# Performance work log

Measured on AMD Instinct MI355X. Metric: run time of the kernel, lower is better.

## Reference

```python
import jax, jax.numpy as jnp
import numpy as np

H = 16      # num_heads
HD = 64     # head_dim
W = 1024    # local window size
G = 256     # number of global tokens
EPS = 1e-6
NEG = -1e30


def setup_inputs() -> dict:
    key = jax.random.key(0)
    ks = jax.random.split(key, 7)
    B, S, D = 1, 8192, 1024
    inner = H * HD
    s = 0.02
    return {
        "x": jax.random.normal(ks[0], (B, S, D), jnp.float32),
        "norm_w": jnp.ones((D,), jnp.float32),
        "w_q": jax.random.normal(ks[1], (D, inner), jnp.float32) * s,
        "w_k": jax.random.normal(ks[2], (D, inner), jnp.float32) * s,
        "w_v": jax.random.normal(ks[3], (D, inner), jnp.float32) * s,
        "w_out": jax.random.normal(ks[4], (inner, D), jnp.float32) * s,
        "scorer_w": jax.random.normal(ks[5], (D, 1), jnp.float32) * s,
        "scorer_b": jnp.zeros((1,), jnp.float32),
    }


def reference(x, norm_w, w_q, w_k, w_v, w_out, scorer_w, scorer_b):
    B, S, D = x.shape
    # pre-norm (RMSNorm)
    h = x * jax.lax.rsqrt(jnp.mean(x * x, axis=-1, keepdims=True) + EPS) * norm_w

    def proj(w):  # [B,S,D] -> [B,H,S,HD]
        return jnp.einsum('bsd,de->bse', h, w).reshape(B, S, H, HD).transpose(0, 2, 1, 3)

    q, k, v = proj(w_q), proj(w_k), proj(w_v)
    scale = HD ** -0.5

    # --- local block attention (non-overlapping causal windows) ---
    nW = S // W
    qw = q.reshape(B, H, nW, W, HD)
    kw = k.reshape(B, H, nW, W, HD)
    vw = v.reshape(B, H, nW, W, HD)
    ll = jnp.einsum('bhnqd,bhnkd->bhnqk', qw, kw) * scale  # [B,H,nW,W,W]
    cm = jnp.tril(jnp.ones((W, W), bool))
    ll = jnp.where(cm, ll, NEG).reshape(B, H, S, W)

    # --- sparse global attention over top-G important tokens ---
    scores = (jnp.einsum('bsd,do->bso', h, scorer_w) + scorer_b)[..., 0]  # [B,S]
    _, idx = jax.lax.top_k(scores, G)                                     # [B,G]
    kg = jnp.take_along_axis(k, idx[:, None, :, None], axis=2)            # [B,H,G,HD]
    vg = jnp.take_along_axis(v, idx[:, None, :, None], axis=2)
    lg = jnp.einsum('bhsd,bhgd->bhsg', q, kg) * scale                     # [B,H,S,G]
    pos = jnp.arange(S)
    gmask = idx[:, None, None, :] <= pos[None, None, :, None]             # causal: global pos <= query pos
    lg = jnp.where(gmask, lg, NEG)

    # --- joint softmax over local window + global tokens ---
    attn = jax.nn.softmax(jnp.concatenate([ll, lg], axis=-1), axis=-1)    # [B,H,S,W+G]
    a_loc = attn[..., :W].reshape(B, H, nW, W, W)
    o = jnp.einsum('bhnqk,bhnkd->bhnqd', a_loc, vw).reshape(B, H, S, HD)
    o = o + jnp.einsum('bhsg,bhgd->bhsd', attn[..., W:], vg)

    o = o.transpose(0, 2, 1, 3).reshape(B, S, H * HD)
    return x + jnp.einsum('bse,ed->bsd', o, w_out)  # residual
```

## Files before the change

kernel.cpp:

```cpp
#include <hip/hip_runtime.h>
#include <stdint.h>

#define S_LEN 8192
#define DIM   1024
#define NH    16
#define HD    64
#define WIN   1024
#define GTOK  256
#define QKV_STRIDE (3 * DIM)

typedef __attribute__((ext_vector_type(8))) short bf16x8;
typedef __attribute__((ext_vector_type(4))) float f32x4;
typedef __attribute__((ext_vector_type(16))) float f32x16;
typedef unsigned short u16;
typedef uint32_t u32;

__device__ __forceinline__ u16 f2bf(float f) {
  union { float f; uint32_t u; } v; v.f = f;
  uint32_t r = v.u + 0x7fffu + ((v.u >> 16) & 1u);
  return (u16)(r >> 16);
}
__device__ __forceinline__ float bf2f(u16 b) {
  union { uint32_t u; float f; } v; v.u = ((uint32_t)b) << 16;
  return v.f;
}
__device__ __forceinline__ uint32_t cvtpk(float a, float b) {
  uint32_t r;
  asm("v_cvt_pk_bf16_f32 %0, %1, %2" : "=v"(r) : "v"(a), "v"(b));
  return r;
}

__device__ __forceinline__ void gload_lds16(const void* g, void* l) {
  __builtin_amdgcn_global_load_lds((const __attribute__((address_space(1))) void*)g,
                                   (__attribute__((address_space(3))) void*)l, 16, 0, 0);
}

__global__ __launch_bounds__(256) void rmsnorm_score_kernel(
    const float* __restrict__ x, const float* __restrict__ nw,
    const float* __restrict__ sw, const float* __restrict__ sb,
    u16* __restrict__ h, float* __restrict__ scores) {
  int row = blockIdx.x, tid = threadIdx.x;
  const float4* xr = (const float4*)(x + (size_t)row * DIM);
  float4 v = xr[tid];
  float ss = v.x * v.x + v.y * v.y + v.z * v.z + v.w * v.w;
#pragma unroll
  for (int o = 32; o >= 1; o >>= 1) ss += __shfl_xor(ss, o);
  __shared__ float red[4], red2[4];
  int wv = tid >> 6;
  if ((tid & 63) == 0) red[wv] = ss;
  __syncthreads();
  ss = red[0] + red[1] + red[2] + red[3];
  float rn = rsqrtf(ss * (1.0f / DIM) + 1e-6f);
  float4 w4 = ((const float4*)nw)[tid];
  float h0 = v.x * rn * w4.x, h1 = v.y * rn * w4.y;
  float h2 = v.z * rn * w4.z, h3 = v.w * rn * w4.w;
  uint64_t pack = (uint64_t)f2bf(h0) | ((uint64_t)f2bf(h1) << 16) |
                  ((uint64_t)f2bf(h2) << 32) | ((uint64_t)f2bf(h3) << 48);
  *(uint64_t*)(h + (size_t)row * DIM + tid * 4) = pack;
  float4 s4 = ((const float4*)sw)[tid];
  float sc = h0 * s4.x + h1 * s4.y + h2 * s4.z + h3 * s4.w;
#pragma unroll
  for (int o = 32; o >= 1; o >>= 1) sc += __shfl_xor(sc, o);
  if ((tid & 63) == 0) red2[wv] = sc;
  __syncthreads();
  if (tid == 0) scores[row] = red2[0] + red2[1] + red2[2] + red2[3] + sb[0];
}

__global__ __launch_bounds__(256) void transpose_w_kernel(
    const float* __restrict__ wq, const float* __restrict__ wk,
    const float* __restrict__ wv, const float* __restrict__ wo,
    u16* __restrict__ wqkvT, u16* __restrict__ woutT) {
  __shared__ float tile[32][33];
  int z = blockIdx.z;
  const float* src = (z == 0) ? wq : (z == 1) ? wk : (z == 2) ? wv : wo;
  u16* dst = (z < 3) ? (wqkvT + (size_t)z * DIM * DIM) : woutT;
  int tx = threadIdx.x, ty = threadIdx.y;
  int n0 = blockIdx.x * 32, k0 = blockIdx.y * 32;
#pragma unroll
  for (int i = 0; i < 4; i++)
    tile[ty + i * 8][tx] = src[(size_t)(k0 + ty + i * 8) * DIM + n0 + tx];
  __syncthreads();
#pragma unroll
  for (int i = 0; i < 4; i++)
    dst[(size_t)(n0 + ty + i * 8) * DIM + k0 + tx] = f2bf(tile[tx][ty + i * 8]);
}

__global__ __launch_bounds__(256) void topk_init_kernel(int* __restrict__ cnt) {
  cnt[blockIdx.x * 256 + threadIdx.x] = 0;
}

__global__ __launch_bounds__(256) void topk_count_kernel(
    const float* __restrict__ scores, int* __restrict__ cnt) {
  __shared__ float sj[1024];
  int jbase = blockIdx.y * 1024;
  for (int t = threadIdx.x; t < 1024; t += 256) sj[t] = scores[jbase + t];
  __syncthreads();
  int i = blockIdx.x * 256 + threadIdx.x;
  float my = scores[i];
  int c = 0;
  const float4* s4 = (const float4*)sj;
#pragma unroll 4
  for (int j = 0; j < 256; j++) {
    float4 v = s4[j];
    int b = jbase + j * 4;
    c += (v.x > my) || (v.x == my && (b + 0) < i);
    c += (v.y > my) || (v.y == my && (b + 1) < i);
    c += (v.z > my) || (v.z == my && (b + 2) < i);
    c += (v.w > my) || (v.w == my && (b + 3) < i);
  }
  if (c) atomicAdd(&cnt[i], c);
}

__global__ __launch_bounds__(256) void topk_scatter_kernel(
    const int* __restrict__ cnt, int* __restrict__ gidx) {
  int i = blockIdx.x * 256 + threadIdx.x;
  int c = cnt[i];
  if (c < GTOK) gidx[c] = i;
}

__global__ __launch_bounds__(128) void gather_kernel(
    const u16* __restrict__ qkv, const int* __restrict__ gidx,
    u16* __restrict__ kg, u16* __restrict__ vg) {
  int g = blockIdx.x, t = threadIdx.x;
  size_t src = (size_t)gidx[g] * QKV_STRIDE;
  *(bf16x8*)(kg + (size_t)g * DIM + t * 8) = *(const bf16x8*)(qkv + src + DIM + t * 8);
  *(bf16x8*)(vg + (size_t)g * DIM + t * 8) = *(const bf16x8*)(qkv + src + 2 * DIM + t * 8);
}

template <int RESID>
__global__ __launch_bounds__(512, 2) void gemm256_kernel(
    const u16* __restrict__ A, const u16* __restrict__ B,
    u16* __restrict__ Cb, float* __restrict__ Cf, const float* __restrict__ X,
    int M, int N, int K) {
  __shared__ __align__(16) u16 As[3][256 * 64];
  __shared__ __align__(16) u16 Bs[3][128 * 64];
  const int tid = threadIdx.x;
  const int wave = tid >> 6, lane = tid & 63;
  const int l15 = lane & 15, l4 = lane >> 4;
  const int wr = wave >> 1, wc = wave & 1;
  const int mbase = blockIdx.x * 256, nbase = blockIdx.y * 128;
  const int srow = lane >> 3, schunk = lane & 7;
  const int gcol = (schunk ^ srow) * 8;

  auto stage = [&](int tt, int b) {
    const int kt = tt << 6;
#pragma unroll
    for (int l = 0; l < 4; l++) {
      int row = wave * 32 + l * 8;
      gload_lds16(A + (size_t)(mbase + row + srow) * K + kt + gcol, &As[b][row * 64]);
    }
#pragma unroll
    for (int l = 0; l < 2; l++) {
      int row = wave * 16 + l * 8;
      gload_lds16(B + (size_t)(nbase + row + srow) * K + kt + gcol, &Bs[b][row * 64]);
    }
  };

  const int nt = K >> 6;
  f32x4 acc[4][4] = {};

  stage(0, 0);
  stage(1, 1);
  asm volatile("s_waitcnt vmcnt(6)" ::: "memory");
  __builtin_amdgcn_s_barrier();
  __builtin_amdgcn_sched_barrier(0);

  int cur = 0;
  for (int t = 0; t < nt; t++) {
    int pre = cur + 2; if (pre >= 3) pre -= 3;
    if (t + 2 < nt) stage(t + 2, pre);
    const u16* Ab = &As[cur][0];
    const u16* Bb = &Bs[cur][0];
    bf16x8 bfr[4][2], af[4][2];
#pragma unroll
    for (int nf = 0; nf < 4; nf++) {
      int row = wc * 64 + nf * 16 + l15;
#pragma unroll
      for (int kk = 0; kk < 2; kk++)
        bfr[nf][kk] = *(const bf16x8*)(Bb + row * 64 + (((kk * 4 + l4) ^ (l15 & 7)) * 8));
    }
#pragma unroll
    for (int mi = 0; mi < 4; mi++) {
      int row = wr * 64 + mi * 16 + l15;
#pragma unroll
      for (int kk = 0; kk < 2; kk++)
        af[mi][kk] = *(const bf16x8*)(Ab + row * 64 + (((kk * 4 + l4) ^ (l15 & 7)) * 8));
    }
    __builtin_amdgcn_s_setprio(1);
#pragma unroll
    for (int mi = 0; mi < 4; mi++)
#pragma unroll
      for (int nf = 0; nf < 4; nf++)
#pragma unroll
        for (int kk = 0; kk < 2; kk++)
          acc[mi][nf] = __builtin_amdgcn_mfma_f32_16x16x32_bf16(af[mi][kk], bfr[nf][kk],
                                                                acc[mi][nf], 0, 0, 0);
    __builtin_amdgcn_s_setprio(0);
    if (t + 1 < nt) {
      if (t + 2 < nt) asm volatile("s_waitcnt vmcnt(6)" ::: "memory");
      else            asm volatile("s_waitcnt vmcnt(0)" ::: "memory");
      __builtin_amdgcn_s_barrier();
      __builtin_amdgcn_sched_barrier(0);
    }
    cur = (cur + 1 == 3) ? 0 : cur + 1;
  }

#pragma unroll
  for (int mi = 0; mi < 4; mi++) {
#pragma unroll
    for (int nf = 0; nf < 4; nf++) {
#pragma unroll
      for (int r = 0; r < 4; r++) {
        int row = mbase + wr * 64 + mi * 16 + l4 * 4 + r;
        int col = nbase + wc * 64 + nf * 16 + l15;
        float v = acc[mi][nf][r];
        if (RESID) Cf[(size_t)row * N + col] = X[(size_t)row * N + col] + v;
        else       Cb[(size_t)row * N + col] = f2bf(v);
      }
    }
  }
}

__global__ __launch_bounds__(512) void attn_kernel(
    const u16* __restrict__ qkv, const u16* __restrict__ kg,
    const u16* __restrict__ vg, const int* __restrict__ gidx,
    u16* __restrict__ o) {
  __shared__ __align__(16) u16 kT[2][64][72];
  __shared__ __align__(16) u16 vT[2][64][72];
  __shared__ int gposLds[2][64];
  const int tid = threadIdx.x, wave = tid >> 6, lane = tid & 63;
  const int l31 = lane & 31, hi = lane >> 5;

  const int r = blockIdx.x + 32 * blockIdx.y;
  const int half = r >> 8, rr = r & 255;
  const int h = rr >> 4, w8 = rr & 7, jj = (rr >> 3) & 1;
  const int j = half ? (jj ? 1 : 0) : (jj ? 2 : 3);
  const int wbase = w8 * WIN;
  const int hoff = h * HD;
  const int qsbase = wbase + j * 256;
  const int nLocal = (j + 1) * 4;
  const int nTiles = nLocal + GTOK / 64;
  const int qrow = qsbase + wave * 32 + l31;
  const int qwmax = qsbase + wave * 32 + 31;

  const int skey = tid >> 3, sd8 = (tid & 7) * 8;
  const int vcol = skey ^ ((sd8 >> 4) << 4);

  bf16x8 qf[4];
  {
    const float SC2 = 0.125f * 1.44269504088896f;
    const u16* qptr = qkv + (size_t)qrow * QKV_STRIDE + hoff + hi * 8;
#pragma unroll
    for (int ks = 0; ks < 4; ks++) {
      bf16x8 raw = *(const bf16x8*)(qptr + ks * 16);
      bf16x8 sc;
#pragma unroll
      for (int t = 0; t < 8; t++) sc[t] = (short)f2bf(bf2f((u16)raw[t]) * SC2);
      qf[ks] = sc;
    }
  }

  bf16x8 nk, nv;
  int ng = 0;
  {
    const u16* base = qkv + (size_t)(wbase + skey) * QKV_STRIDE + hoff + sd8;
    nk = *(const bf16x8*)(base + DIM);
    nv = *(const bf16x8*)(base + 2 * DIM);
  }

  f32x16 acc0 = {}, acc1 = {};
  float mr = -3.0e38f, lr = 0.f;

  for (int t = 0; t < nTiles; t++) {
    const int p = t & 1;
    const bool isLocal = (t < nLocal);
    const int tbase = wbase + t * 64;
    *(bf16x8*)(&kT[p][skey][sd8]) = nk;
#pragma unroll
    for (int t8 = 0; t8 < 8; t8++) vT[p][sd8 + t8][vcol] = (u16)nv[t8];
    if (!isLocal && tid < 64) gposLds[p][tid] = ng;
    {
      const int nt = t + 1;
      const u16 *ksrc = nullptr, *vsrc = nullptr;
      if (nt < nLocal) {
        const u16* base = qkv + (size_t)(wbase + nt * 64 + skey) * QKV_STRIDE + hoff + sd8;
        ksrc = base + DIM; vsrc = base + 2 * DIM;
      } else if (nt < nTiles) {
        size_t grow = (size_t)((nt - nLocal) * 64 + skey) * DIM + hoff + sd8;
        ksrc = kg + grow; vsrc = vg + grow;
        if (tid < 64) ng = gidx[(nt - nLocal) * 64 + tid];
      }
      if (ksrc) { nk = *(const bf16x8*)(ksrc); nv = *(const bf16x8*)(vsrc); }
    }
    asm volatile("s_waitcnt lgkmcnt(0)" ::: "memory");
    __builtin_amdgcn_s_barrier();
    __builtin_amdgcn_sched_barrier(0);

    if (isLocal && tbase > qwmax) continue;

    float sv[32];
    __builtin_amdgcn_s_setprio(1);
#pragma unroll
    for (int kb = 0; kb < 2; kb++) {
      const u16* krow = &kT[p][kb * 32 + l31][hi * 8];
      bf16x8 k0 = *(const bf16x8*)(krow);
      bf16x8 k1 = *(const bf16x8*)(krow + 16);
      bf16x8 k2 = *(const bf16x8*)(krow + 32);
      bf16x8 k3 = *(const bf16x8*)(krow + 48);
      f32x16 z = {};
      z = __builtin_amdgcn_mfma_f32_32x32x16_bf16(k0, qf[0], z, 0, 0, 0);
      z = __builtin_amdgcn_mfma_f32_32x32x16_bf16(k1, qf[1], z, 0, 0, 0);
      z = __builtin_amdgcn_mfma_f32_32x32x16_bf16(k2, qf[2], z, 0, 0, 0);
      z = __builtin_amdgcn_mfma_f32_32x32x16_bf16(k3, qf[3], z, 0, 0, 0);
#pragma unroll
      for (int rg = 0; rg < 16; rg++) sv[kb * 16 + rg] = z[rg];
    }
    __builtin_amdgcn_s_setprio(0);

    if (isLocal) {
      const int lim = qrow - tbase;
      if (lim < 63) {
#pragma unroll
        for (int kb = 0; kb < 2; kb++)
#pragma unroll
          for (int rg = 0; rg < 16; rg++) {
            int crow = kb * 32 + (rg & 3) + 8 * (rg >> 2) + 4 * hi;
            if (crow > lim) sv[kb * 16 + rg] = -3.0e38f;
          }
      }
    } else {
#pragma unroll
      for (int kb = 0; kb < 2; kb++)
#pragma unroll
        for (int rg = 0; rg < 16; rg++) {
          int kpos = gposLds[p][kb * 32 + (rg & 3) + 8 * (rg >> 2) + 4 * hi];
          if (kpos > qrow) sv[kb * 16 + rg] = -3.0e38f;
        }
    }

    float m0 = sv[0], m1 = sv[1], m2 = sv[2], m3 = sv[3];
#pragma unroll
    for (int i = 4; i < 32; i += 4) {
      m0 = fmaxf(m0, sv[i]);     m1 = fmaxf(m1, sv[i + 1]);
      m2 = fmaxf(m2, sv[i + 2]); m3 = fmaxf(m3, sv[i + 3]);
    }
    float vmax = fmaxf(fmaxf(m0, m1), fmaxf(m2, m3));
    vmax = fmaxf(vmax, __shfl_xor(vmax, 32));
    if (__any(vmax > mr + 11.0f)) {
      float mn = fmaxf(mr, vmax);
      float al = exp2f(mr - mn);
      lr *= al;
      mr = mn;
#pragma unroll
      for (int i = 0; i < 16; i++) { acc0[i] *= al; acc1[i] *= al; }
    }
    float s0 = 0.f, s1 = 0.f, s2 = 0.f, s3 = 0.f;
#pragma unroll
    for (int i = 0; i < 32; i += 4) {
      float p0 = exp2f(sv[i] - mr),     p1 = exp2f(sv[i + 1] - mr);
      float p2 = exp2f(sv[i + 2] - mr), p3 = exp2f(sv[i + 3] - mr);
      sv[i] = p0; sv[i + 1] = p1; sv[i + 2] = p2; sv[i + 3] = p3;
      s0 += p0; s1 += p1; s2 += p2; s3 += p3;
    }
    float ps = (s0 + s1) + (s2 + s3);
    ps += __shfl_xor(ps, 32);
    lr += ps;

    bf16x8 pf[4];
#pragma unroll
    for (int q4 = 0; q4 < 4; q4++) {
      int b = q4 * 8;
      uint32_t w0 = cvtpk(sv[b + 0], sv[b + 1]);
      uint32_t w1 = cvtpk(sv[b + 2], sv[b + 3]);
      uint32_t w2 = cvtpk(sv[b + 4], sv[b + 5]);
      uint32_t w3 = cvtpk(sv[b + 6], sv[b + 7]);
      uint32_t w0s = __shfl_xor((int)w0, 32), w2s = __shfl_xor((int)w2, 32);
      uint32_t w1s = __shfl_xor((int)w1, 32), w3s = __shfl_xor((int)w3, 32);
      union { uint32_t w[4]; bf16x8 v; } u;
      u.w[0] = hi ? w2s : w0;
      u.w[1] = hi ? w3s : w1;
      u.w[2] = hi ? w2 : w0s;
      u.w[3] = hi ? w3 : w1s;
      pf[q4] = u.v;
    }

    __builtin_amdgcn_s_setprio(1);
#pragma unroll
    for (int dblk = 0; dblk < 2; dblk++) {
      const int swz = (dblk * 2 + (l31 >> 4)) << 4;
      const u16* vrow = &vT[p][dblk * 32 + l31][0];
      f32x16 a = dblk ? acc1 : acc0;
#pragma unroll
      for (int ksg = 0; ksg < 4; ksg++) {
        bf16x8 vf = *(const bf16x8*)(vrow + ((ksg * 16 + hi * 8) ^ swz));
        a = __builtin_amdgcn_mfma_f32_32x32x16_bf16(vf, pf[ksg], a, 0, 0, 0);
      }
      if (dblk) acc1 = a; else acc0 = a;
    }
    __builtin_amdgcn_s_setprio(0);
  }

  float inv = 1.0f / lr;
#pragma unroll
  for (int dblk = 0; dblk < 2; dblk++) {
    f32x16 a = dblk ? acc1 : acc0;
#pragma unroll
    for (int g = 0; g < 4; g++) {
      uint64_t pk = (uint64_t)f2bf(a[g * 4 + 0] * inv)
                  | ((uint64_t)f2bf(a[g * 4 + 1] * inv) << 16)
                  | ((uint64_t)f2bf(a[g * 4 + 2] * inv) << 32)
                  | ((uint64_t)f2bf(a[g * 4 + 3] * inv) << 48);
      *(uint64_t*)(o + (size_t)qrow * DIM + hoff + dblk * 32 + g * 8 + 4 * hi) = pk;
    }
  }
}

extern "C" void kernel_launch(void* const* d_in, const int* in_sizes, int n_in,
                              void* d_out, int out_size, void* d_ws, size_t ws_size,
                              hipStream_t stream) {
  const float* x  = (const float*)d_in[0];
  const float* nw = (const float*)d_in[1];
  const float* wq = (const float*)d_in[2];
  const float* wk = (const float*)d_in[3];
  const float* wv = (const float*)d_in[4];
  const float* wo = (const float*)d_in[5];
  const float* sw = (const float*)d_in[6];
  const float* sb = (const float*)d_in[7];
  float* out = (float*)d_out;

  char* ws = (char*)d_ws;
  size_t off = 0;
  auto alloc = [&](size_t b) {
    char* p = ws + off;
    off = (off + b + 255) & ~(size_t)255;
    return p;
  };
  u16*   h      = (u16*)alloc((size_t)S_LEN * DIM * 2);
  u16*   wqkvT  = (u16*)alloc((size_t)3 * DIM * DIM * 2);
  u16*   woutT  = (u16*)alloc((size_t)DIM * DIM * 2);
  u16*   qkv    = (u16*)alloc((size_t)S_LEN * 3 * DIM * 2);
  u16*   obuf   = (u16*)alloc((size_t)S_LEN * DIM * 2);
  float* scores = (float*)alloc((size_t)S_LEN * 4);
  int*   gidx   = (int*)alloc((size_t)GTOK * 4);
  int*   cnt    = (int*)alloc((size_t)S_LEN * 4);
  u16*   kgbuf  = (u16*)alloc((size_t)GTOK * DIM * 2);
  u16*   vgbuf  = (u16*)alloc((size_t)GTOK * DIM * 2);

  transpose_w_kernel<<<dim3(32, 32, 4), dim3(32, 8), 0, stream>>>(wq, wk, wv, wo, wqkvT, woutT);
  rmsnorm_score_kernel<<<dim3(S_LEN), dim3(256), 0, stream>>>(x, nw, sw, sb, h, scores);
  topk_init_kernel<<<dim3(S_LEN / 256), dim3(256), 0, stream>>>(cnt);
  topk_count_kernel<<<dim3(32, 8), dim3(256), 0, stream>>>(scores, cnt);
  topk_scatter_kernel<<<dim3(S_LEN / 256), dim3(256), 0, stream>>>(cnt, gidx);
  gemm256_kernel<0><<<dim3(32, 24), dim3(512), 0, stream>>>(h, wqkvT, qkv, nullptr, nullptr,
                                                            S_LEN, 3 * DIM, DIM);
  gather_kernel<<<dim3(GTOK), dim3(128), 0, stream>>>(qkv, gidx, kgbuf, vgbuf);
  attn_kernel<<<dim3(32, NH), dim3(512), 0, stream>>>(qkv, kgbuf, vgbuf, gidx, obuf);
  gemm256_kernel<1><<<dim3(32, 8), dim3(512), 0, stream>>>(obuf, woutT, nullptr, out, x,
                                                           S_LEN, DIM, DIM);
}
```

Baseline: 228.6 us.

## Sort global tokens by position to skip causally masked global tiles

```diff
diff --git a/kernel.cpp b/kernel.cpp
--- a/kernel.cpp
+++ b/kernel.cpp
@@ -85,8 +85,8 @@
     dst[(size_t)(n0 + ty + i * 8) * DIM + k0 + tx] = f2bf(tile[tx][ty + i * 8]);
 }
 
-__global__ __launch_bounds__(256) void topk_init_kernel(int* __restrict__ cnt) {
-  cnt[blockIdx.x * 256 + threadIdx.x] = 0;
+__global__ __launch_bounds__(256) void zero_kernel(int* __restrict__ p) {
+  p[blockIdx.x * 256 + threadIdx.x] = 0;
 }
 
 __global__ __launch_bounds__(256) void topk_count_kernel(
@@ -111,11 +111,30 @@
   if (c) atomicAdd(&cnt[i], c);
 }
 
-__global__ __launch_bounds__(256) void topk_scatter_kernel(
-    const int* __restrict__ cnt, int* __restrict__ gidx) {
+__global__ __launch_bounds__(256) void selrank_kernel(
+    const int* __restrict__ cnt, int* __restrict__ scnt) {
+  __shared__ int sj[1024];
+  int jbase = blockIdx.y * 1024;
+  for (int t = threadIdx.x; t < 1024; t += 256) sj[t] = (cnt[jbase + t] < GTOK);
+  __syncthreads();
   int i = blockIdx.x * 256 + threadIdx.x;
-  int c = cnt[i];
-  if (c < GTOK) gidx[c] = i;
+  if (cnt[i] >= GTOK) return;
+  int c = 0;
+  const int4* s4 = (const int4*)sj;
+#pragma unroll 4
+  for (int j = 0; j < 256; j++) {
+    int4 v = s4[j];
+    int b = jbase + j * 4;
+    c += (v.x && (b + 0) < i) + (v.y && (b + 1) < i) +
+         (v.z && (b + 2) < i) + (v.w && (b + 3) < i);
+  }
+  if (c) atomicAdd(&scnt[i], c);
+}
+
+__global__ __launch_bounds__(256) void selscatter_kernel(
+    const int* __restrict__ cnt, const int* __restrict__ scnt, int* __restrict__ gidxS) {
+  int i = blockIdx.x * 256 + threadIdx.x;
+  if (cnt[i] < GTOK) gidxS[scnt[i]] = i;
 }
 
 __global__ __launch_bounds__(128) void gather_kernel(
@@ -138,20 +157,23 @@
   const int wave = tid >> 6, lane = tid & 63;
   const int l15 = lane & 15, l4 = lane >> 4;
   const int wr = wave >> 1, wc = wave & 1;
-  const int mbase = blockIdx.x * 256, nbase = blockIdx.y * 128;
+  const int nwg = gridDim.x * gridDim.y;
+  const int l = blockIdx.x + (blockIdx.y << 5);
+  const int sw = (l & 7) * (nwg >> 3) + (l >> 3);
+  const int mbase = (sw & 31) * 256, nbase = (sw >> 5) * 128;
   const int srow = lane >> 3, schunk = lane & 7;
   const int gcol = (schunk ^ srow) * 8;
 
   auto stage = [&](int tt, int b) {
     const int kt = tt << 6;
 #pragma unroll
-    for (int l = 0; l < 4; l++) {
-      int row = wave * 32 + l * 8;
+    for (int q = 0; q < 4; q++) {
+      int row = wave * 32 + q * 8;
       gload_lds16(A + (size_t)(mbase + row + srow) * K + kt + gcol, &As[b][row * 64]);
     }
 #pragma unroll
-    for (int l = 0; l < 2; l++) {
-      int row = wave * 16 + l * 8;
+    for (int q = 0; q < 2; q++) {
+      int row = wave * 16 + q * 8;
       gload_lds16(B + (size_t)(nbase + row + srow) * K + kt + gcol, &Bs[b][row * 64]);
     }
   };
@@ -221,7 +243,7 @@
   }
 }
 
-__global__ __launch_bounds__(512) void attn_kernel(
+__global__ __launch_bounds__(512, 4) void attn_kernel(
     const u16* __restrict__ qkv, const u16* __restrict__ kg,
     const u16* __restrict__ vg, const int* __restrict__ gidx,
     u16* __restrict__ o) {
@@ -239,7 +261,11 @@
   const int hoff = h * HD;
   const int qsbase = wbase + j * 256;
   const int nLocal = (j + 1) * 4;
-  const int nTiles = nLocal + GTOK / 64;
+  const int qsmax = qsbase + 255;
+  int gcount = 0;
+#pragma unroll
+  for (int g = 0; g < 4; g++) gcount += (gidx[g * 64] <= qsmax) ? 1 : 0;
+  const int nTiles = nLocal + gcount;
   const int qrow = qsbase + wave * 32 + l31;
   const int qwmax = qsbase + wave * 32 + 31;
 
@@ -296,7 +322,11 @@
     __builtin_amdgcn_s_barrier();
     __builtin_amdgcn_sched_barrier(0);
 
-    if (isLocal && tbase > qwmax) continue;
+    if (isLocal) {
+      if (tbase > qwmax) continue;
+    } else {
+      if (gposLds[p][0] > qwmax) continue;
+    }
 
     float sv[32];
     __builtin_amdgcn_s_setprio(1);
@@ -441,20 +471,23 @@
   u16*   qkv    = (u16*)alloc((size_t)S_LEN * 3 * DIM * 2);
   u16*   obuf   = (u16*)alloc((size_t)S_LEN * DIM * 2);
   float* scores = (float*)alloc((size_t)S_LEN * 4);
-  int*   gidx   = (int*)alloc((size_t)GTOK * 4);
   int*   cnt    = (int*)alloc((size_t)S_LEN * 4);
+  int*   scnt   = (int*)alloc((size_t)S_LEN * 4);
+  int*   gidxS  = (int*)alloc((size_t)GTOK * 4);
   u16*   kgbuf  = (u16*)alloc((size_t)GTOK * DIM * 2);
   u16*   vgbuf  = (u16*)alloc((size_t)GTOK * DIM * 2);
 
   transpose_w_kernel<<<dim3(32, 32, 4), dim3(32, 8), 0, stream>>>(wq, wk, wv, wo, wqkvT, woutT);
   rmsnorm_score_kernel<<<dim3(S_LEN), dim3(256), 0, stream>>>(x, nw, sw, sb, h, scores);
-  topk_init_kernel<<<dim3(S_LEN / 256), dim3(256), 0, stream>>>(cnt);
+  zero_kernel<<<dim3(S_LEN / 256), dim3(256), 0, stream>>>(cnt);
+  zero_kernel<<<dim3(S_LEN / 256), dim3(256), 0, stream>>>(scnt);
   topk_count_kernel<<<dim3(32, 8), dim3(256), 0, stream>>>(scores, cnt);
-  topk_scatter_kernel<<<dim3(S_LEN / 256), dim3(256), 0, stream>>>(cnt, gidx);
+  selrank_kernel<<<dim3(32, 8), dim3(256), 0, stream>>>(cnt, scnt);
+  selscatter_kernel<<<dim3(S_LEN / 256), dim3(256), 0, stream>>>(cnt, scnt, gidxS);
   gemm256_kernel<0><<<dim3(32, 24), dim3(512), 0, stream>>>(h, wqkvT, qkv, nullptr, nullptr,
                                                             S_LEN, 3 * DIM, DIM);
-  gather_kernel<<<dim3(GTOK), dim3(128), 0, stream>>>(qkv, gidx, kgbuf, vgbuf);
-  attn_kernel<<<dim3(32, NH), dim3(512), 0, stream>>>(qkv, kgbuf, vgbuf, gidx, obuf);
+  gather_kernel<<<dim3(GTOK), dim3(128), 0, stream>>>(qkv, gidxS, kgbuf, vgbuf);
+  attn_kernel<<<dim3(32, NH), dim3(512), 0, stream>>>(qkv, kgbuf, vgbuf, gidxS, obuf);
   gemm256_kernel<1><<<dim3(32, 8), dim3(512), 0, stream>>>(obuf, woutT, nullptr, out, x,
                                                            S_LEN, DIM, DIM);
 }
```

Result: slower. 290.1 us (+26.9%).

## Pair attention query blocks per workgroup and fold topk counter init into rmsnorm

Applied to the files above, without the earlier changes.

```diff
diff --git a/kernel.cpp b/kernel.cpp
--- a/kernel.cpp
+++ b/kernel.cpp
@@ -38,7 +38,7 @@
 __global__ __launch_bounds__(256) void rmsnorm_score_kernel(
     const float* __restrict__ x, const float* __restrict__ nw,
     const float* __restrict__ sw, const float* __restrict__ sb,
-    u16* __restrict__ h, float* __restrict__ scores) {
+    u16* __restrict__ h, float* __restrict__ scores, int* __restrict__ cnt) {
   int row = blockIdx.x, tid = threadIdx.x;
   const float4* xr = (const float4*)(x + (size_t)row * DIM);
   float4 v = xr[tid];
@@ -63,7 +63,10 @@
   for (int o = 32; o >= 1; o >>= 1) sc += __shfl_xor(sc, o);
   if ((tid & 63) == 0) red2[wv] = sc;
   __syncthreads();
-  if (tid == 0) scores[row] = red2[0] + red2[1] + red2[2] + red2[3] + sb[0];
+  if (tid == 0) {
+    scores[row] = red2[0] + red2[1] + red2[2] + red2[3] + sb[0];
+    cnt[row] = 0;
+  }
 }
 
 __global__ __launch_bounds__(256) void transpose_w_kernel(
@@ -83,10 +86,6 @@
 #pragma unroll
   for (int i = 0; i < 4; i++)
     dst[(size_t)(n0 + ty + i * 8) * DIM + k0 + tx] = f2bf(tile[tx][ty + i * 8]);
-}
-
-__global__ __launch_bounds__(256) void topk_init_kernel(int* __restrict__ cnt) {
-  cnt[blockIdx.x * 256 + threadIdx.x] = 0;
 }
 
 __global__ __launch_bounds__(256) void topk_count_kernel(
@@ -145,13 +144,13 @@
   auto stage = [&](int tt, int b) {
     const int kt = tt << 6;
 #pragma unroll
-    for (int l = 0; l < 4; l++) {
-      int row = wave * 32 + l * 8;
+    for (int q = 0; q < 4; q++) {
+      int row = wave * 32 + q * 8;
       gload_lds16(A + (size_t)(mbase + row + srow) * K + kt + gcol, &As[b][row * 64]);
     }
 #pragma unroll
-    for (int l = 0; l < 2; l++) {
-      int row = wave * 16 + l * 8;
+    for (int q = 0; q < 2; q++) {
+      int row = wave * 16 + q * 8;
       gload_lds16(B + (size_t)(nbase + row + srow) * K + kt + gcol, &Bs[b][row * 64]);
     }
   };
@@ -225,40 +224,17 @@
     const u16* __restrict__ qkv, const u16* __restrict__ kg,
     const u16* __restrict__ vg, const int* __restrict__ gidx,
     u16* __restrict__ o) {
-  __shared__ __align__(16) u16 kT[2][64][72];
-  __shared__ __align__(16) u16 vT[2][64][72];
+  __shared__ u16 kT[2][64][72];
+  __shared__ u16 vT[2][64][72];
   __shared__ int gposLds[2][64];
   const int tid = threadIdx.x, wave = tid >> 6, lane = tid & 63;
   const int l31 = lane & 31, hi = lane >> 5;
-
-  const int r = blockIdx.x + 32 * blockIdx.y;
-  const int half = r >> 8, rr = r & 255;
-  const int h = rr >> 4, w8 = rr & 7, jj = (rr >> 3) & 1;
-  const int j = half ? (jj ? 1 : 0) : (jj ? 2 : 3);
-  const int wbase = w8 * WIN;
-  const int hoff = h * HD;
-  const int qsbase = wbase + j * 256;
-  const int nLocal = (j + 1) * 4;
-  const int nTiles = nLocal + GTOK / 64;
-  const int qrow = qsbase + wave * 32 + l31;
-  const int qwmax = qsbase + wave * 32 + 31;
+  const int win = blockIdx.x >> 1, pair = blockIdx.x & 1;
+  const int wbase = win * WIN;
+  const int hoff = blockIdx.y * HD;
 
   const int skey = tid >> 3, sd8 = (tid & 7) * 8;
   const int vcol = skey ^ ((sd8 >> 4) << 4);
-
-  bf16x8 qf[4];
-  {
-    const float SC2 = 0.125f * 1.44269504088896f;
-    const u16* qptr = qkv + (size_t)qrow * QKV_STRIDE + hoff + hi * 8;
-#pragma unroll
-    for (int ks = 0; ks < 4; ks++) {
-      bf16x8 raw = *(const bf16x8*)(qptr + ks * 16);
-      bf16x8 sc;
-#pragma unroll
-      for (int t = 0; t < 8; t++) sc[t] = (short)f2bf(bf2f((u16)raw[t]) * SC2);
-      qf[ks] = sc;
-    }
-  }
 
   bf16x8 nk, nv;
   int ng = 0;
@@ -268,149 +244,175 @@
     nv = *(const bf16x8*)(base + 2 * DIM);
   }
 
-  f32x16 acc0 = {}, acc1 = {};
-  float mr = -3.0e38f, lr = 0.f;
-
-  for (int t = 0; t < nTiles; t++) {
-    const int p = t & 1;
-    const bool isLocal = (t < nLocal);
-    const int tbase = wbase + t * 64;
-    *(bf16x8*)(&kT[p][skey][sd8]) = nk;
-#pragma unroll
-    for (int t8 = 0; t8 < 8; t8++) vT[p][sd8 + t8][vcol] = (u16)nv[t8];
-    if (!isLocal && tid < 64) gposLds[p][tid] = ng;
+  for (int sp = 0; sp < 2; sp++) {
+    const int j = sp ? (3 - pair) : pair;
+    const int qsbase = wbase + j * 256;
+    const int nLocal = (j + 1) * 4;
+    const int nTiles = nLocal + GTOK / 64;
+    const int qrow = qsbase + wave * 32 + l31;
+    const int qwmax = qsbase + wave * 32 + 31;
+
+    bf16x8 qf[4];
     {
-      const int nt = t + 1;
-      const u16 *ksrc = nullptr, *vsrc = nullptr;
-      if (nt < nLocal) {
-        const u16* base = qkv + (size_t)(wbase + nt * 64 + skey) * QKV_STRIDE + hoff + sd8;
-        ksrc = base + DIM; vsrc = base + 2 * DIM;
-      } else if (nt < nTiles) {
-        size_t grow = (size_t)((nt - nLocal) * 64 + skey) * DIM + hoff + sd8;
-        ksrc = kg + grow; vsrc = vg + grow;
-        if (tid < 64) ng = gidx[(nt - nLocal) * 64 + tid];
-      }
-      if (ksrc) { nk = *(const bf16x8*)(ksrc); nv = *(const bf16x8*)(vsrc); }
-    }
-    asm volatile("s_waitcnt lgkmcnt(0)" ::: "memory");
-    __builtin_amdgcn_s_barrier();
-    __builtin_amdgcn_sched_barrier(0);
-
-    if (isLocal && tbase > qwmax) continue;
-
-    float sv[32];
-    __builtin_amdgcn_s_setprio(1);
-#pragma unroll
-    for (int kb = 0; kb < 2; kb++) {
-      const u16* krow = &kT[p][kb * 32 + l31][hi * 8];
-      bf16x8 k0 = *(const bf16x8*)(krow);
-      bf16x8 k1 = *(const bf16x8*)(krow + 16);
-      bf16x8 k2 = *(const bf16x8*)(krow + 32);
-      bf16x8 k3 = *(const bf16x8*)(krow + 48);
-      f32x16 z = {};
-      z = __builtin_amdgcn_mfma_f32_32x32x16_bf16(k0, qf[0], z, 0, 0, 0);
-      z = __builtin_amdgcn_mfma_f32_32x32x16_bf16(k1, qf[1], z, 0, 0, 0);
-      z = __builtin_amdgcn_mfma_f32_32x32x16_bf16(k2, qf[2], z, 0, 0, 0);
-      z = __builtin_amdgcn_mfma_f32_32x32x16_bf16(k3, qf[3], z, 0, 0, 0);
-#pragma unroll
-      for (int rg = 0; rg < 16; rg++) sv[kb * 16 + rg] = z[rg];
-    }
-    __builtin_amdgcn_s_setprio(0);
-
-    if (isLocal) {
-      const int lim = qrow - tbase;
-      if (lim < 63) {
+      const float SC2 = 0.125f * 1.44269504088896f;
+      const u16* qptr = qkv + (size_t)qrow * QKV_STRIDE + hoff + hi * 8;
+#pragma unroll
+      for (int ks = 0; ks < 4; ks++) {
+        bf16x8 raw = *(const bf16x8*)(qptr + ks * 16);
+        bf16x8 sc;
+#pragma unroll
+        for (int jj = 0; jj < 8; jj++) sc[jj] = (short)f2bf(bf2f((u16)raw[jj]) * SC2);
+        qf[ks] = sc;
+      }
+    }
+
+    f32x16 acc0 = {}, acc1 = {};
+    float mr = -3.0e38f, lr = 0.f;
+
+    __syncthreads();
+
+    for (int t = 0; t < nTiles; t++) {
+      const int p = t & 1;
+      const bool isLocal = (t < nLocal);
+      const int tbase = wbase + t * 64;
+      *(bf16x8*)(&kT[p][skey][sd8]) = nk;
+#pragma unroll
+      for (int jj = 0; jj < 8; jj++) vT[p][sd8 + jj][vcol] = (u16)nv[jj];
+      if (!isLocal && tid < 64) gposLds[p][tid] = ng;
+      {
+        const int nt = t + 1;
+        const u16 *ksrc = nullptr, *vsrc = nullptr;
+        if (nt < nLocal) {
+          const u16* base = qkv + (size_t)(wbase + nt * 64 + skey) * QKV_STRIDE + hoff + sd8;
+          ksrc = base + DIM; vsrc = base + 2 * DIM;
+        } else if (nt < nTiles) {
+          size_t grow = (size_t)((nt - nLocal) * 64 + skey) * DIM + hoff + sd8;
+          ksrc = kg + grow; vsrc = vg + grow;
+          if (tid < 64) ng = gidx[(nt - nLocal) * 64 + tid];
+        } else if (sp == 0) {
+          const u16* base = qkv + (size_t)(wbase + skey) * QKV_STRIDE + hoff + sd8;
+          ksrc = base + DIM; vsrc = base + 2 * DIM;
+        }
+        if (ksrc) { nk = *(const bf16x8*)(ksrc); nv = *(const bf16x8*)(vsrc); }
+      }
+      __syncthreads();
+
+      if (isLocal && tbase > qwmax) continue;
+
+      float sv[32];
+      __builtin_amdgcn_s_setprio(1);
+#pragma unroll
+      for (int kb = 0; kb < 2; kb++) {
+        const u16* krow = &kT[p][kb * 32 + l31][hi * 8];
+        bf16x8 k0 = *(const bf16x8*)(krow);
+        bf16x8 k1 = *(const bf16x8*)(krow + 16);
+        bf16x8 k2 = *(const bf16x8*)(krow + 32);
+        bf16x8 k3 = *(const bf16x8*)(krow + 48);
+        f32x16 z = {};
+        z = __builtin_amdgcn_mfma_f32_32x32x16_bf16(k0, qf[0], z, 0, 0, 0);
+        z = __builtin_amdgcn_mfma_f32_32x32x16_bf16(k1, qf[1], z, 0, 0, 0);
+        z = __builtin_amdgcn_mfma_f32_32x32x16_bf16(k2, qf[2], z, 0, 0, 0);
+        z = __builtin_amdgcn_mfma_f32_32x32x16_bf16(k3, qf[3], z, 0, 0, 0);
+#pragma unroll
+        for (int r = 0; r < 16; r++) sv[kb * 16 + r] = z[r];
+      }
+      __builtin_amdgcn_s_setprio(0);
+
+      if (isLocal) {
+        const int lim = qrow - tbase;
+        if (lim < 63) {
+#pragma unroll
+          for (int kb = 0; kb < 2; kb++)
+#pragma unroll
+            for (int r = 0; r < 16; r++) {
+              int crow = kb * 32 + (r & 3) + 8 * (r >> 2) + 4 * hi;
+              if (crow > lim) sv[kb * 16 + r] = -3.0e38f;
+            }
+        }
+      } else {
 #pragma unroll
         for (int kb = 0; kb < 2; kb++)
 #pragma unroll
-          for (int rg = 0; rg < 16; rg++) {
-            int crow = kb * 32 + (rg & 3) + 8 * (rg >> 2) + 4 * hi;
-            if (crow > lim) sv[kb * 16 + rg] = -3.0e38f;
+          for (int r = 0; r < 16; r++) {
+            int kpos = gposLds[p][kb * 32 + (r & 3) + 8 * (r >> 2) + 4 * hi];
+            if (kpos > qrow) sv[kb * 16 + r] = -3.0e38f;
           }
       }
-    } else {
-#pragma unroll
-      for (int kb = 0; kb < 2; kb++)
-#pragma unroll
-        for (int rg = 0; rg < 16; rg++) {
-          int kpos = gposLds[p][kb * 32 + (rg & 3) + 8 * (rg >> 2) + 4 * hi];
-          if (kpos > qrow) sv[kb * 16 + rg] = -3.0e38f;
+
+      float m0 = sv[0], m1 = sv[1], m2 = sv[2], m3 = sv[3];
+#pragma unroll
+      for (int i = 4; i < 32; i += 4) {
+        m0 = fmaxf(m0, sv[i]);     m1 = fmaxf(m1, sv[i + 1]);
+        m2 = fmaxf(m2, sv[i + 2]); m3 = fmaxf(m3, sv[i + 3]);
+      }
+      float vmax = fmaxf(fmaxf(m0, m1), fmaxf(m2, m3));
+      vmax = fmaxf(vmax, __shfl_xor(vmax, 32));
+      if (__any(vmax > mr + 11.0f)) {
+        float mn = fmaxf(mr, vmax);
+        float al = exp2f(mr - mn);
+        lr *= al;
+        mr = mn;
+#pragma unroll
+        for (int i = 0; i < 16; i++) { acc0[i] *= al; acc1[i] *= al; }
+      }
+      float s0 = 0.f, s1 = 0.f, s2 = 0.f, s3 = 0.f;
+#pragma unroll
+      for (int i = 0; i < 32; i += 4) {
+        float p0 = exp2f(sv[i] - mr),     p1 = exp2f(sv[i + 1] - mr);
+        float p2 = exp2f(sv[i + 2] - mr), p3 = exp2f(sv[i + 3] - mr);
+        sv[i] = p0; sv[i + 1] = p1; sv[i + 2] = p2; sv[i + 3] = p3;
+        s0 += p0; s1 += p1; s2 += p2; s3 += p3;
+      }
+      float ps = (s0 + s1) + (s2 + s3);
+      ps += __shfl_xor(ps, 32);
+      lr += ps;
+
+      bf16x8 pf[4];
+#pragma unroll
+      for (int q4 = 0; q4 < 4; q4++) {
+        int b = q4 * 8;
+        uint32_t w0 = cvtpk(sv[b + 0], sv[b + 1]);
+        uint32_t w1 = cvtpk(sv[b + 2], sv[b + 3]);
+        uint32_t w2 = cvtpk(sv[b + 4], sv[b + 5]);
+        uint32_t w3 = cvtpk(sv[b + 6], sv[b + 7]);
+        uint32_t w0s = __shfl_xor((int)w0, 32), w2s = __shfl_xor((int)w2, 32);
+        uint32_t w1s = __shfl_xor((int)w1, 32), w3s = __shfl_xor((int)w3, 32);
+        union { uint32_t w[4]; bf16x8 v; } u;
+        u.w[0] = hi ? w2s : w0;
+        u.w[1] = hi ? w3s : w1;
+        u.w[2] = hi ? w2 : w0s;
+        u.w[3] = hi ? w3 : w1s;
+        pf[q4] = u.v;
+      }
+
+      __builtin_amdgcn_s_setprio(1);
+#pragma unroll
+      for (int dblk = 0; dblk < 2; dblk++) {
+        const int swz = (dblk * 2 + (l31 >> 4)) << 4;
+        const u16* vrow = &vT[p][dblk * 32 + l31][0];
+        f32x16 a = dblk ? acc1 : acc0;
+#pragma unroll
+        for (int ksg = 0; ksg < 4; ksg++) {
+          bf16x8 vf = *(const bf16x8*)(vrow + ((ksg * 16 + hi * 8) ^ swz));
+          a = __builtin_amdgcn_mfma_f32_32x32x16_bf16(vf, pf[ksg], a, 0, 0, 0);
         }
-    }
-
-    float m0 = sv[0], m1 = sv[1], m2 = sv[2], m3 = sv[3];
-#pragma unroll
-    for (int i = 4; i < 32; i += 4) {
-      m0 = fmaxf(m0, sv[i]);     m1 = fmaxf(m1, sv[i + 1]);
-      m2 = fmaxf(m2, sv[i + 2]); m3 = fmaxf(m3, sv[i + 3]);
-    }
-    float vmax = fmaxf(fmaxf(m0, m1), fmaxf(m2, m3));
-    vmax = fmaxf(vmax, __shfl_xor(vmax, 32));
-    if (__any(vmax > mr + 11.0f)) {
-      float mn = fmaxf(mr, vmax);
-      float al = exp2f(mr - mn);
-      lr *= al;
-      mr = mn;
-#pragma unroll
-      for (int i = 0; i < 16; i++) { acc0[i] *= al; acc1[i] *= al; }
-    }
-    float s0 = 0.f, s1 = 0.f, s2 = 0.f, s3 = 0.f;
-#pragma unroll
-    for (int i = 0; i < 32; i += 4) {
-      float p0 = exp2f(sv[i] - mr),     p1 = exp2f(sv[i + 1] - mr);
-      float p2 = exp2f(sv[i + 2] - mr), p3 = exp2f(sv[i + 3] - mr);
-      sv[i] = p0; sv[i + 1] = p1; sv[i + 2] = p2; sv[i + 3] = p3;
-      s0 += p0; s1 += p1; s2 += p2; s3 += p3;
-    }
-    float ps = (s0 + s1) + (s2 + s3);
-    ps += __shfl_xor(ps, 32);
-    lr += ps;
-
-    bf16x8 pf[4];
-#pragma unroll
-    for (int q4 = 0; q4 < 4; q4++) {
-      int b = q4 * 8;
-      uint32_t w0 = cvtpk(sv[b + 0], sv[b + 1]);
-      uint32_t w1 = cvtpk(sv[b + 2], sv[b + 3]);
-      uint32_t w2 = cvtpk(sv[b + 4], sv[b + 5]);
-      uint32_t w3 = cvtpk(sv[b + 6], sv[b + 7]);
-      uint32_t w0s = __shfl_xor((int)w0, 32), w2s = __shfl_xor((int)w2, 32);
-      uint32_t w1s = __shfl_xor((int)w1, 32), w3s = __shfl_xor((int)w3, 32);
-      union { uint32_t w[4]; bf16x8 v; } u;
-      u.w[0] = hi ? w2s : w0;
-      u.w[1] = hi ? w3s : w1;
-      u.w[2] = hi ? w2 : w0s;
-      u.w[3] = hi ? w3 : w1s;
-      pf[q4] = u.v;
-    }
-
-    __builtin_amdgcn_s_setprio(1);
+        if (dblk) acc1 = a; else acc0 = a;
+      }
+      __builtin_amdgcn_s_setprio(0);
+    }
+
+    float inv = 1.0f / lr;
 #pragma unroll
     for (int dblk = 0; dblk < 2; dblk++) {
-      const int swz = (dblk * 2 + (l31 >> 4)) << 4;
-      const u16* vrow = &vT[p][dblk * 32 + l31][0];
       f32x16 a = dblk ? acc1 : acc0;
 #pragma unroll
-      for (int ksg = 0; ksg < 4; ksg++) {
-        bf16x8 vf = *(const bf16x8*)(vrow + ((ksg * 16 + hi * 8) ^ swz));
-        a = __builtin_amdgcn_mfma_f32_32x32x16_bf16(vf, pf[ksg], a, 0, 0, 0);
-      }
-      if (dblk) acc1 = a; else acc0 = a;
-    }
-    __builtin_amdgcn_s_setprio(0);
-  }
-
-  float inv = 1.0f / lr;
-#pragma unroll
-  for (int dblk = 0; dblk < 2; dblk++) {
-    f32x16 a = dblk ? acc1 : acc0;
-#pragma unroll
-    for (int g = 0; g < 4; g++) {
-      uint64_t pk = (uint64_t)f2bf(a[g * 4 + 0] * inv)
-                  | ((uint64_t)f2bf(a[g * 4 + 1] * inv) << 16)
-                  | ((uint64_t)f2bf(a[g * 4 + 2] * inv) << 32)
-                  | ((uint64_t)f2bf(a[g * 4 + 3] * inv) << 48);
-      *(uint64_t*)(o + (size_t)qrow * DIM + hoff + dblk * 32 + g * 8 + 4 * hi) = pk;
+      for (int g = 0; g < 4; g++) {
+        uint64_t pk = (uint64_t)f2bf(a[g * 4 + 0] * inv)
+                    | ((uint64_t)f2bf(a[g * 4 + 1] * inv) << 16)
+                    | ((uint64_t)f2bf(a[g * 4 + 2] * inv) << 32)
+                    | ((uint64_t)f2bf(a[g * 4 + 3] * inv) << 48);
+        *(uint64_t*)(o + (size_t)qrow * DIM + hoff + dblk * 32 + g * 8 + 4 * hi) = pk;
+      }
     }
   }
 }
@@ -441,20 +443,19 @@
   u16*   qkv    = (u16*)alloc((size_t)S_LEN * 3 * DIM * 2);
   u16*   obuf   = (u16*)alloc((size_t)S_LEN * DIM * 2);
   float* scores = (float*)alloc((size_t)S_LEN * 4);
+  int*   cnt    = (int*)alloc((size_t)S_LEN * 4);
   int*   gidx   = (int*)alloc((size_t)GTOK * 4);
-  int*   cnt    = (int*)alloc((size_t)S_LEN * 4);
   u16*   kgbuf  = (u16*)alloc((size_t)GTOK * DIM * 2);
   u16*   vgbuf  = (u16*)alloc((size_t)GTOK * DIM * 2);
 
   transpose_w_kernel<<<dim3(32, 32, 4), dim3(32, 8), 0, stream>>>(wq, wk, wv, wo, wqkvT, woutT);
-  rmsnorm_score_kernel<<<dim3(S_LEN), dim3(256), 0, stream>>>(x, nw, sw, sb, h, scores);
-  topk_init_kernel<<<dim3(S_LEN / 256), dim3(256), 0, stream>>>(cnt);
+  rmsnorm_score_kernel<<<dim3(S_LEN), dim3(256), 0, stream>>>(x, nw, sw, sb, h, scores, cnt);
   topk_count_kernel<<<dim3(32, 8), dim3(256), 0, stream>>>(scores, cnt);
   topk_scatter_kernel<<<dim3(S_LEN / 256), dim3(256), 0, stream>>>(cnt, gidx);
   gemm256_kernel<0><<<dim3(32, 24), dim3(512), 0, stream>>>(h, wqkvT, qkv, nullptr, nullptr,
                                                             S_LEN, 3 * DIM, DIM);
   gather_kernel<<<dim3(GTOK), dim3(128), 0, stream>>>(qkv, gidx, kgbuf, vgbuf);
-  attn_kernel<<<dim3(32, NH), dim3(512), 0, stream>>>(qkv, kgbuf, vgbuf, gidx, obuf);
+  attn_kernel<<<dim3(16, NH), dim3(512), 0, stream>>>(qkv, kgbuf, vgbuf, gidx, obuf);
   gemm256_kernel<1><<<dim3(32, 8), dim3(512), 0, stream>>>(obuf, woutT, nullptr, out, x,
                                                            S_LEN, DIM, DIM);
 }
```

New measurement: 219.8 us. -3.9%, faster.
